# Optimization experiments

Hardware: AMD Instinct MI355X
Metric: run time of the kernel (lower is better)

Reference implementation:

```python
import jax, jax.numpy as jnp
import numpy as np

HINGE_VALUE = 1.0

def setup_inputs() -> dict:
    key = jax.random.key(0)
    k1, k2 = jax.random.split(key)
    x_pred = jax.random.normal(k1, (8192, 128), dtype=jnp.float32)
    x_target = jax.random.normal(k2, (16384, 128), dtype=jnp.float32)
    return {"x_pred": x_pred, "x_target": x_target, "top_k": 5}


def _cdist(a, b):
    # Euclidean distance via GEMM form: ||a||^2 + ||b||^2 - 2 a.b
    a2 = jnp.sum(a * a, axis=-1, keepdims=True)          # [N,1]
    b2 = jnp.sum(b * b, axis=-1, keepdims=True).T        # [1,M]
    d2 = a2 + b2 - 2.0 * (a @ b.T)                       # [N,M]
    return jnp.sqrt(jnp.maximum(d2, 0.0))


def reference(x_pred, x_target, top_k):
    c_dist = _cdist(x_pred, x_target)                    # [N,M]
    # smallest-k distances per pred point
    neg_vals, _ = jax.lax.top_k(-c_dist, top_k)          # [N,k]
    values = jnp.maximum(-neg_vals - HINGE_VALUE, 0.0)   # hinge
    return jnp.mean(values)
```

## Files before the change

### kernel.cpp

```cpp
#include <hip/hip_runtime.h>
#include <hip/hip_bf16.h>
#include <float.h>

#define N_PRED 8192
#define M_TGT  16384
#define KD     128
#define TOPK   5
#define SPLITS 8
#define MSPLIT (M_TGT / SPLITS)
#define TILE_T 64
#define NTILES (MSPLIT / TILE_T)
#define ROWS_PER_BLOCK 256
#define ROWBLKS (N_PRED / ROWS_PER_BLOCK)

using short8  = __attribute__((ext_vector_type(8))) short;
using floatx4 = __attribute__((ext_vector_type(4))) float;

__device__ __forceinline__ unsigned short f2bf(float v) {
    unsigned int u = __float_as_uint(v);
    u = (u + 0x7FFFu + ((u >> 16) & 1u)) >> 16;
    return (unsigned short)u;
}

__device__ __forceinline__ void async16(const void* g, void* l) {
    __builtin_amdgcn_global_load_lds(
        (const __attribute__((address_space(1))) unsigned int*)g,
        (__attribute__((address_space(3))) unsigned int*)l, 16, 0, 0);
}
__device__ __forceinline__ void async4(const void* g, void* l) {
    __builtin_amdgcn_global_load_lds(
        (const __attribute__((address_space(1))) unsigned int*)g,
        (__attribute__((address_space(3))) unsigned int*)l, 4, 0, 0);
}

__device__ __forceinline__ void ins5(float* t, float d) {
    t[4] = __builtin_amdgcn_fmed3f(d, t[3], t[4]);
    t[3] = __builtin_amdgcn_fmed3f(d, t[2], t[3]);
    t[2] = __builtin_amdgcn_fmed3f(d, t[1], t[2]);
    t[1] = __builtin_amdgcn_fmed3f(d, t[0], t[1]);
    t[0] = fminf(t[0], d);
}

__global__ void prep_kernel(const float* __restrict__ pred,
                            const float* __restrict__ tgt,
                            unsigned short* __restrict__ predB,
                            unsigned short* __restrict__ tgtB,
                            float* __restrict__ a2,
                            float* __restrict__ b2,
                            float* __restrict__ acc,
                            unsigned int* __restrict__ counter) {
    const int row = blockIdx.x * 8 + (threadIdx.x >> 5);
    const int l32 = threadIdx.x & 31;
    const float* src;
    unsigned short* dst;
    float scale;
    float* norm;
    if (row < N_PRED) {
        src = pred + (size_t)row * KD;
        dst = predB + (size_t)row * KD;
        scale = -2.0f;
        norm = a2 + row;
    } else {
        const int rr = row - N_PRED;
        src = tgt + (size_t)rr * KD;
        dst = tgtB + (size_t)rr * KD;
        scale = 1.0f;
        norm = b2 + rr;
    }
    const float4 x = reinterpret_cast<const float4*>(src)[l32];
    uint2 p;
    p.x = (unsigned int)f2bf(x.x * scale) | ((unsigned int)f2bf(x.y * scale) << 16);
    p.y = (unsigned int)f2bf(x.z * scale) | ((unsigned int)f2bf(x.w * scale) << 16);
    reinterpret_cast<uint2*>(dst)[l32] = p;
    float s = x.x * x.x + x.y * x.y + x.z * x.z + x.w * x.w;
    #pragma unroll
    for (int off = 16; off > 0; off >>= 1) s += __shfl_down(s, off, 32);
    if (l32 == 0) norm[0] = s;
    if (blockIdx.x == 0 && threadIdx.x == 0) { acc[0] = 0.0f; counter[0] = 0u; }
}

__global__ __launch_bounds__(512, 2) void density_kernel(
        const unsigned short* __restrict__ predB,
        const unsigned short* __restrict__ tgtB,
        const float* __restrict__ b2,
        float* __restrict__ wsTop) {
    const int tid   = threadIdx.x;
    const int wave  = tid >> 6;
    const int lane  = tid & 63;
    const int col   = lane & 15;
    const int quad  = lane >> 4;
    const int split = blockIdx.x & (SPLITS - 1);
    const int rowblk = blockIdx.x >> 3;
    const int r0 = rowblk * ROWS_PER_BLOCK + wave * 32;
    const int m0 = split * MSPLIT;

    __shared__ short8 frag[2][TILE_T * 16];
    __shared__ float  b2s[2][TILE_T];

    short8 afrag[2][4];
    #pragma unroll
    for (int rf = 0; rf < 2; rf++)
        #pragma unroll
        for (int kf = 0; kf < 4; kf++)
            afrag[rf][kf] = *reinterpret_cast<const short8*>(
                predB + (size_t)(r0 + rf * 16 + col) * KD + kf * 32 + quad * 8);

    float t5[2][4][5];
    #pragma unroll
    for (int rf = 0; rf < 2; rf++)
        #pragma unroll
        for (int rg = 0; rg < 4; rg++)
            #pragma unroll
            for (int j = 0; j < 5; j++)
                t5[rf][rg][j] = FLT_MAX;

    {
        const int m0t = m0;
        #pragma unroll
        for (int s = 0; s < 2; ++s) {
            const int ci = wave * 2 + s, g = ci >> 2, kf = ci & 3;
            const unsigned short* src =
                tgtB + (size_t)(m0t + g * 16 + col) * KD + kf * 32 + quad * 8;
            async16(src, &frag[0][ci * 64]);
        }
        if (wave == 0) async4(b2 + m0t + lane, &b2s[0][0]);
    }
    __syncthreads();

    for (int t = 0; t < NTILES; ++t) {
        const int cur = t & 1;
        if (t + 1 < NTILES) {
            const int m0t = m0 + (t + 1) * TILE_T;
            #pragma unroll
            for (int s = 0; s < 2; ++s) {
                const int ci = wave * 2 + s, g = ci >> 2, kf = ci & 3;
                const unsigned short* src =
                    tgtB + (size_t)(m0t + g * 16 + col) * KD + kf * 32 + quad * 8;
                async16(src, &frag[cur ^ 1][ci * 64]);
            }
            if (wave == 0) async4(b2 + m0t + lane, &b2s[cur ^ 1][0]);
        }

        #pragma unroll
        for (int g = 0; g < 4; ++g) {
            const float bq = b2s[cur][g * 16 + col];
            short8 bf[4];
            #pragma unroll
            for (int kf = 0; kf < 4; ++kf)
                bf[kf] = frag[cur][(g * 4 + kf) * 64 + lane];
            #pragma unroll
            for (int rf = 0; rf < 2; ++rf) {
                floatx4 c = {bq, bq, bq, bq};
                c = __builtin_amdgcn_mfma_f32_16x16x32_bf16(afrag[rf][0], bf[0], c, 0, 0, 0);
                c = __builtin_amdgcn_mfma_f32_16x16x32_bf16(afrag[rf][1], bf[1], c, 0, 0, 0);
                c = __builtin_amdgcn_mfma_f32_16x16x32_bf16(afrag[rf][2], bf[2], c, 0, 0, 0);
                c = __builtin_amdgcn_mfma_f32_16x16x32_bf16(afrag[rf][3], bf[3], c, 0, 0, 0);
                #pragma unroll
                for (int rg = 0; rg < 4; ++rg) ins5(t5[rf][rg], c[rg]);
            }
        }
        __syncthreads();
    }

    #pragma unroll
    for (int off = 1; off < 16; off <<= 1) {
        #pragma unroll
        for (int rf = 0; rf < 2; ++rf)
            #pragma unroll
            for (int rg = 0; rg < 4; ++rg) {
                float o0 = __shfl_xor(t5[rf][rg][0], off);
                float o1 = __shfl_xor(t5[rf][rg][1], off);
                float o2 = __shfl_xor(t5[rf][rg][2], off);
                float o3 = __shfl_xor(t5[rf][rg][3], off);
                float o4 = __shfl_xor(t5[rf][rg][4], off);
                ins5(t5[rf][rg], o0); ins5(t5[rf][rg], o1); ins5(t5[rf][rg], o2);
                ins5(t5[rf][rg], o3); ins5(t5[rf][rg], o4);
            }
    }

    if (col == 0) {
        #pragma unroll
        for (int rf = 0; rf < 2; ++rf)
            #pragma unroll
            for (int rg = 0; rg < 4; ++rg) {
                const int row = r0 + rf * 16 + quad * 4 + rg;
                float* dst = wsTop + ((size_t)row * SPLITS + split) * 5;
                #pragma unroll
                for (int j = 0; j < 5; ++j) dst[j] = t5[rf][rg][j];
            }
    }
}

__global__ void merge_kernel(const float* __restrict__ wsTop,
                             const float* __restrict__ a2,
                             float* __restrict__ acc,
                             unsigned int* __restrict__ counter,
                             float* __restrict__ out) {
    const int row = blockIdx.x * 256 + threadIdx.x;
    const float* p = wsTop + (size_t)row * (SPLITS * 5);
    float u[5] = {FLT_MAX, FLT_MAX, FLT_MAX, FLT_MAX, FLT_MAX};
    #pragma unroll
    for (int i = 0; i < SPLITS * 5; ++i) ins5(u, p[i]);
    const float a = a2[row];
    float hs = 0.0f;
    #pragma unroll
    for (int j = 0; j < 5; ++j) {
        const float dd = sqrtf(fmaxf(u[j] + a, 0.0f));
        hs += fmaxf(dd - 1.0f, 0.0f);
    }
    #pragma unroll
    for (int off = 32; off > 0; off >>= 1) hs += __shfl_down(hs, off);
    __shared__ float ws[4];
    if ((threadIdx.x & 63) == 0) ws[threadIdx.x >> 6] = hs;
    __syncthreads();
    if (threadIdx.x == 0) {
        atomicAdd(acc, ws[0] + ws[1] + ws[2] + ws[3]);
        __threadfence();
        const unsigned int done = atomicAdd(counter, 1u);
        if (done == gridDim.x - 1) {
            const float tot = atomicAdd(acc, 0.0f);
            out[0] = tot * (1.0f / (float)(N_PRED * TOPK));
        }
    }
}

extern "C" void kernel_launch(void* const* d_in, const int* in_sizes, int n_in,
                              void* d_out, int out_size, void* d_ws, size_t ws_size,
                              hipStream_t stream) {
    const float* pred = (const float*)d_in[0];
    const float* tgt  = (const float*)d_in[1];
    char* ws = (char*)d_ws;
    unsigned short* predB = (unsigned short*)(ws);
    unsigned short* tgtB  = (unsigned short*)(ws + (size_t)2 * 1024 * 1024);
    float* a2   = (float*)(ws + (size_t)6 * 1024 * 1024);
    float* b2   = (float*)(ws + (size_t)6 * 1024 * 1024 + 32 * 1024);
    float* acc  = (float*)(ws + (size_t)6 * 1024 * 1024 + 96 * 1024);
    unsigned int* counter = (unsigned int*)(ws + (size_t)6 * 1024 * 1024 + 96 * 1024 + 64);
    float* wsTop = (float*)(ws + (size_t)7 * 1024 * 1024);
    float* out = (float*)d_out;

    prep_kernel<<<(N_PRED + M_TGT) / 8, 256, 0, stream>>>(pred, tgt, predB, tgtB, a2, b2, acc, counter);
    density_kernel<<<ROWBLKS * SPLITS, 512, 0, stream>>>(predB, tgtB, b2, wsTop);
    merge_kernel<<<N_PRED / 256, 256, 0, stream>>>(wsTop, a2, acc, counter, out);
}
```

Before: 134.7 us.

## Fuse merge into density kernel, triple-buffer tiles, double splits

Doubles the target-dimension splits to 16, giving 512 blocks instead of 256 for better CU occupancy. Replaces the double-buffered LDS pipeline with a three-stage one that uses explicit vmcnt waits and raw barriers. Removes the separate merge kernel: the last-arriving split block for each row block merges the partial top-5 results and accumulates the total into a double atomic. This saves a launch and adds more partial top-k merging, plus counter and atomic contention.

Result: slower. 159.8 us (+18.6%).

```diff
diff --git a/kernel.cpp b/kernel.cpp
--- a/kernel.cpp
+++ b/kernel.cpp
@@ -6,7 +6,7 @@
 #define M_TGT  16384
 #define KD     128
 #define TOPK   5
-#define SPLITS 8
+#define SPLITS 16
 #define MSPLIT (M_TGT / SPLITS)
 #define TILE_T 64
 #define NTILES (MSPLIT / TILE_T)
@@ -47,8 +47,8 @@
                             unsigned short* __restrict__ tgtB,
                             float* __restrict__ a2,
                             float* __restrict__ b2,
-                            float* __restrict__ acc,
-                            unsigned int* __restrict__ counter) {
+                            double* __restrict__ acc,
+                            unsigned int* __restrict__ counters) {
     const int row = blockIdx.x * 8 + (threadIdx.x >> 5);
     const int l32 = threadIdx.x & 31;
     const float* src;
@@ -76,26 +76,33 @@
     #pragma unroll
     for (int off = 16; off > 0; off >>= 1) s += __shfl_down(s, off, 32);
     if (l32 == 0) norm[0] = s;
-    if (blockIdx.x == 0 && threadIdx.x == 0) { acc[0] = 0.0f; counter[0] = 0u; }
+    if (blockIdx.x == 0) {
+        if (threadIdx.x == 0) acc[0] = 0.0;
+        if (threadIdx.x < ROWBLKS + 1) counters[threadIdx.x] = 0u;
+    }
 }
 
 __global__ __launch_bounds__(512, 2) void density_kernel(
         const unsigned short* __restrict__ predB,
         const unsigned short* __restrict__ tgtB,
         const float* __restrict__ b2,
-        float* __restrict__ wsTop) {
+        const float* __restrict__ a2,
+        float* __restrict__ wsTop,
+        double* __restrict__ acc,
+        unsigned int* __restrict__ counters,
+        float* __restrict__ out) {
     const int tid   = threadIdx.x;
     const int wave  = tid >> 6;
     const int lane  = tid & 63;
     const int col   = lane & 15;
     const int quad  = lane >> 4;
     const int split = blockIdx.x & (SPLITS - 1);
-    const int rowblk = blockIdx.x >> 3;
+    const int rowblk = blockIdx.x >> 4;
     const int r0 = rowblk * ROWS_PER_BLOCK + wave * 32;
     const int m0 = split * MSPLIT;
 
-    __shared__ short8 frag[2][TILE_T * 16];
-    __shared__ float  b2s[2][TILE_T];
+    __shared__ short8 frag[3][TILE_T * 16];
+    __shared__ float  b2s[3][TILE_T];
 
     short8 afrag[2][4];
     #pragma unroll
@@ -114,32 +121,27 @@
             for (int j = 0; j < 5; j++)
                 t5[rf][rg][j] = FLT_MAX;
 
-    {
-        const int m0t = m0;
+    auto stage = [&](int t, int buf) {
+        const int m0t = m0 + t * TILE_T;
         #pragma unroll
         for (int s = 0; s < 2; ++s) {
             const int ci = wave * 2 + s, g = ci >> 2, kf = ci & 3;
             const unsigned short* src =
                 tgtB + (size_t)(m0t + g * 16 + col) * KD + kf * 32 + quad * 8;
-            async16(src, &frag[0][ci * 64]);
-        }
-        if (wave == 0) async4(b2 + m0t + lane, &b2s[0][0]);
-    }
-    __syncthreads();
+            async16(src, &frag[buf][ci * 64]);
+        }
+        async4(b2 + m0t + lane, &b2s[buf][0]);
+    };
+
+    stage(0, 0);
+    stage(1, 1);
+    asm volatile("s_waitcnt vmcnt(3)" ::: "memory");
+    __builtin_amdgcn_s_barrier();
+    asm volatile("" ::: "memory");
 
     for (int t = 0; t < NTILES; ++t) {
-        const int cur = t & 1;
-        if (t + 1 < NTILES) {
-            const int m0t = m0 + (t + 1) * TILE_T;
-            #pragma unroll
-            for (int s = 0; s < 2; ++s) {
-                const int ci = wave * 2 + s, g = ci >> 2, kf = ci & 3;
-                const unsigned short* src =
-                    tgtB + (size_t)(m0t + g * 16 + col) * KD + kf * 32 + quad * 8;
-                async16(src, &frag[cur ^ 1][ci * 64]);
-            }
-            if (wave == 0) async4(b2 + m0t + lane, &b2s[cur ^ 1][0]);
-        }
+        const int cur = t % 3;
+        if (t + 2 < NTILES) stage(t + 2, (t + 2) % 3);
 
         #pragma unroll
         for (int g = 0; g < 4; ++g) {
@@ -159,7 +161,13 @@
                 for (int rg = 0; rg < 4; ++rg) ins5(t5[rf][rg], c[rg]);
             }
         }
-        __syncthreads();
+
+        if (t < NTILES - 1) {
+            if (t < NTILES - 2) asm volatile("s_waitcnt vmcnt(3)" ::: "memory");
+            else                asm volatile("s_waitcnt vmcnt(0)" ::: "memory");
+            __builtin_amdgcn_s_barrier();
+            asm volatile("" ::: "memory");
+        }
     }
 
     #pragma unroll
@@ -189,37 +197,43 @@
                 for (int j = 0; j < 5; ++j) dst[j] = t5[rf][rg][j];
             }
     }
-}
-
-__global__ void merge_kernel(const float* __restrict__ wsTop,
-                             const float* __restrict__ a2,
-                             float* __restrict__ acc,
-                             unsigned int* __restrict__ counter,
-                             float* __restrict__ out) {
-    const int row = blockIdx.x * 256 + threadIdx.x;
-    const float* p = wsTop + (size_t)row * (SPLITS * 5);
-    float u[5] = {FLT_MAX, FLT_MAX, FLT_MAX, FLT_MAX, FLT_MAX};
-    #pragma unroll
-    for (int i = 0; i < SPLITS * 5; ++i) ins5(u, p[i]);
-    const float a = a2[row];
-    float hs = 0.0f;
-    #pragma unroll
-    for (int j = 0; j < 5; ++j) {
-        const float dd = sqrtf(fmaxf(u[j] + a, 0.0f));
-        hs += fmaxf(dd - 1.0f, 0.0f);
-    }
-    #pragma unroll
-    for (int off = 32; off > 0; off >>= 1) hs += __shfl_down(hs, off);
-    __shared__ float ws[4];
-    if ((threadIdx.x & 63) == 0) ws[threadIdx.x >> 6] = hs;
+
     __syncthreads();
-    if (threadIdx.x == 0) {
-        atomicAdd(acc, ws[0] + ws[1] + ws[2] + ws[3]);
+    __shared__ unsigned int doMerge;
+    if (tid == 0) {
         __threadfence();
-        const unsigned int done = atomicAdd(counter, 1u);
-        if (done == gridDim.x - 1) {
-            const float tot = atomicAdd(acc, 0.0f);
-            out[0] = tot * (1.0f / (float)(N_PRED * TOPK));
+        doMerge = (atomicAdd(&counters[rowblk], 1u) == SPLITS - 1) ? 1u : 0u;
+    }
+    __syncthreads();
+    if (doMerge) {
+        float hs = 0.0f;
+        if (tid < ROWS_PER_BLOCK) {
+            const int row = rowblk * ROWS_PER_BLOCK + tid;
+            const float* p = wsTop + (size_t)row * (SPLITS * 5);
+            float u[5] = {FLT_MAX, FLT_MAX, FLT_MAX, FLT_MAX, FLT_MAX};
+            for (int i = 0; i < SPLITS * 5; ++i) ins5(u, p[i]);
+            const float a = a2[row];
+            #pragma unroll
+            for (int j = 0; j < 5; ++j) {
+                const float dd = sqrtf(fmaxf(u[j] + a, 0.0f));
+                hs += fmaxf(dd - 1.0f, 0.0f);
+            }
+        }
+        #pragma unroll
+        for (int off = 32; off > 0; off >>= 1) hs += __shfl_down(hs, off);
+        __shared__ float wsum[8];
+        if (lane == 0) wsum[wave] = hs;
+        __syncthreads();
+        if (tid == 0) {
+            float bs = 0.0f;
+            #pragma unroll
+            for (int w = 0; w < 8; ++w) bs += wsum[w];
+            atomicAdd(acc, (double)bs);
+            __threadfence();
+            if (atomicAdd(&counters[ROWBLKS], 1u) == ROWBLKS - 1) {
+                const double tot = atomicAdd(acc, 0.0);
+                out[0] = (float)(tot * (1.0 / (double)(N_PRED * TOPK)));
+            }
         }
     }
 }
@@ -234,12 +248,11 @@
     unsigned short* tgtB  = (unsigned short*)(ws + (size_t)2 * 1024 * 1024);
     float* a2   = (float*)(ws + (size_t)6 * 1024 * 1024);
     float* b2   = (float*)(ws + (size_t)6 * 1024 * 1024 + 32 * 1024);
-    float* acc  = (float*)(ws + (size_t)6 * 1024 * 1024 + 96 * 1024);
-    unsigned int* counter = (unsigned int*)(ws + (size_t)6 * 1024 * 1024 + 96 * 1024 + 64);
-    float* wsTop = (float*)(ws + (size_t)7 * 1024 * 1024);
+    double* acc = (double*)(ws + (size_t)6 * 1024 * 1024 + 96 * 1024);
+    unsigned int* counters = (unsigned int*)(ws + (size_t)6 * 1024 * 1024 + 96 * 1024 + 64);
+    float* wsTop = (float*)(ws + (size_t)6 * 1024 * 1024 + 128 * 1024);
     float* out = (float*)d_out;
 
-    prep_kernel<<<(N_PRED + M_TGT) / 8, 256, 0, stream>>>(pred, tgt, predB, tgtB, a2, b2, acc, counter);
-    density_kernel<<<ROWBLKS * SPLITS, 512, 0, stream>>>(predB, tgtB, b2, wsTop);
-    merge_kernel<<<N_PRED / 256, 256, 0, stream>>>(wsTop, a2, acc, counter, out);
-}
+    prep_kernel<<<(N_PRED + M_TGT) / 8, 256, 0, stream>>>(pred, tgt, predB, tgtB, a2, b2, acc, counters);
+    density_kernel<<<ROWBLKS * SPLITS, 512, 0, stream>>>(predB, tgtB, b2, a2, wsTop, acc, counters, out);
+}
```
